# Optimization experiments

Hardware: AMD Instinct MI355X
Metric: run time of the kernel (lower is better)

Reference implementation:

```python
import jax, jax.numpy as jnp
import numpy as np

B = 256          # batch of molecules
N_ATOM = 1024    # atoms per molecule
N_EDGE = 8192    # directed edges per molecule (avg degree 8)
NEG_SLOPE = 0.01 # torch LeakyReLU default


def setup_inputs() -> dict:
    key = jax.random.key(0)
    ks = jax.random.split(key, 8)
    x = jax.random.normal(ks[0], (B, 3 * N_ATOM), dtype=jnp.float32)
    edge_index = jax.random.randint(ks[1], (2, N_EDGE), 0, N_ATOM, dtype=jnp.int64)
    # GCNConv weights (Glorot-ish small scale) and biases
    W1 = jax.random.normal(ks[2], (3, 64), dtype=jnp.float32) * 0.3
    b1 = jnp.zeros((64,), jnp.float32)
    W2 = jax.random.normal(ks[3], (64, 64), dtype=jnp.float32) * 0.1
    b2 = jnp.zeros((64,), jnp.float32)
    # project MLP: Linear(64,128) + LeakyReLU
    Wp = jax.random.normal(ks[4], (64, 128), dtype=jnp.float32) * 0.1
    bp = jnp.zeros((128,), jnp.float32)
    return {"x": x, "edge_index": edge_index, "W1": W1, "b1": b1,
            "W2": W2, "b2": b2, "Wp": Wp, "bp": bp}


def _leaky_relu(v):
    return jnp.where(v >= 0, v, NEG_SLOPE * v)


def reference(x, edge_index, W1, b1, W2, b2, Wp, bp):
    # x: [B, 3*n_atom] -> node features [B, n_atom, 3]
    bsz, n_feat = x.shape
    n = n_feat // 3
    h = x.reshape(bsz, n, 3)

    src = edge_index[0]  # message sources
    dst = edge_index[1]  # aggregation targets

    # GCN normalization with self-loops: deg[i] = 1 + in-degree(i)
    ones_e = jnp.ones((src.shape[0],), x.dtype)
    deg = jax.ops.segment_sum(ones_e, dst, num_segments=n) + 1.0
    dinv = jax.lax.rsqrt(deg)                # deg^{-1/2}, deg >= 1
    norm_e = dinv[src] * dinv[dst]           # [E]
    norm_self = dinv * dinv                  # self-loop weight per node

    def gcn(h, W, b):
        hw = h @ W                                        # [B, n, d_out]
        msg = hw[:, src, :] * norm_e[None, :, None]       # [B, E, d_out]
        agg = jax.vmap(lambda m: jax.ops.segment_sum(m, dst, num_segments=n))(msg)
        return agg + norm_self[None, :, None] * hw + b

    h = _leaky_relu(gcn(h, W1, b1))
    h = _leaky_relu(gcn(h, W2, b2))

    # global_mean_pool: every graph has exactly n atoms -> mean over atom axis
    g = h.mean(axis=1)                                    # [B, 64]

    # project MLP: Linear + LeakyReLU
    return _leaky_relu(g @ Wp + bp)                       # [B, 128]
```

## Files before the change

kernel.cpp:

```cpp
#include <hip/hip_runtime.h>

#define N_ATOMS 1024
#define N_EDGES 8192
#define NBATCH  256
#define NEG     0.01f

typedef unsigned int u32;
typedef __attribute__((ext_vector_type(2))) float f32x2;
typedef __attribute__((ext_vector_type(4))) float f32x4;
typedef __attribute__((ext_vector_type(8))) _Float16 f16x8;

__device__ __forceinline__ u32 pkrtz(float lo, float hi) {
    u32 r;
    asm("v_cvt_pkrtz_f16_f32 %0, %1, %2" : "=v"(r) : "v"(lo), "v"(hi));
    return r;
}
#define FMIX_LO(a, w, u) \
    asm("v_fma_mix_f32 %0, %1, %2, %0 op_sel_hi:[0,1,0]" : "+v"(a) : "v"(w), "v"(u))
#define FMIX_HI(a, w, u) \
    asm("v_fma_mix_f32 %0, %1, %2, %0 op_sel:[0,1,0] op_sel_hi:[0,1,0]" : "+v"(a) : "v"(w), "v"(u))

#define ROWPTR_OFF 0
#define COLW_OFF   4352
#define SELFW_OFF  (4352 + 73728)
#define PERM_OFF   (SELFW_OFF + 4096)
#define W2T_OFF    (PERM_OFF + 4096)

#define TSTR_B 144
#define SM_TILE_BYTES (N_ATOMS * TSTR_B)
#define SM_AUX_OFF SM_TILE_BYTES
#define SM_TOTAL (SM_TILE_BYTES + 12288)

__global__ __launch_bounds__(1024) void build_csr(
    const int* __restrict__ ei,
    int*  __restrict__ rowptr,
    int2* __restrict__ colw,
    float* __restrict__ selfw_g,
    int*  __restrict__ perm_g,
    u32*  __restrict__ w2t,
    const float* __restrict__ W2)
{
    __shared__ int   sdeg[N_ATOMS];
    __shared__ int   sstart[N_ATOMS];
    __shared__ float sdinv[N_ATOMS];
    __shared__ int   wtot[16];
    __shared__ int   hist[128];
    const int t = threadIdx.x;
    const int lane = t & 63;
    const int w = t >> 6;
    const int* srcA = ei;
    const int* dstA = ei + N_EDGES;

    sdeg[t] = 0;
    if (t < 128) hist[t] = 0;
    __syncthreads();
    for (int e = t; e < N_EDGES; e += 1024) atomicAdd(&sdeg[dstA[e]], 1);
    __syncthreads();

    const int deg  = sdeg[t];
    const int pdeg = (deg + 1) & ~1;
    int v = pdeg;
    #pragma unroll
    for (int d = 1; d < 64; d <<= 1) {
        int u = __shfl_up(v, d, 64);
        if (lane >= d) v += u;
    }
    if (lane == 63) wtot[w] = v;
    __syncthreads();
    if (t == 0) {
        int run = 0;
        #pragma unroll
        for (int i = 0; i < 16; ++i) { int c = wtot[i]; wtot[i] = run; run += c; }
    }
    __syncthreads();
    const int start = v - pdeg + wtot[w];
    sstart[t] = start;
    const float dv = rsqrtf((float)deg + 1.0f);
    sdinv[t] = dv;
    rowptr[t] = start;
    if (t == N_ATOMS - 1) rowptr[N_ATOMS] = start + pdeg;
    selfw_g[t] = dv * dv;
    if (deg & 1) colw[start + deg] = make_int2(0, 0);

    #pragma unroll
    for (int i = 0; i < 2; ++i) {
        const int idx = t + i * 1024;
        const int c = idx >> 5, kk = idx & 31;
        w2t[c * 32 + kk] = pkrtz(W2[(2 * kk) * 64 + c], W2[(2 * kk + 1) * 64 + c]);
    }

    const int dcl = deg < 127 ? deg : 127;
    atomicAdd(&hist[dcl], 1);
    sdeg[t] = 0;
    __syncthreads();
    if (t == 0) {
        int run = 0;
        for (int i = 0; i < 128; ++i) { int c = hist[i]; hist[i] = run; run += c; }
    }
    __syncthreads();
    const int pos = atomicAdd(&hist[dcl], 1);
    perm_g[pos] = t;
    __syncthreads();

    for (int e = t; e < N_EDGES; e += 1024) {
        const int d = dstA[e];
        const int s = srcA[e];
        const int slot = atomicAdd(&sdeg[d], 1);
        const float wgt = sdinv[s] * sdinv[d];
        colw[sstart[d] + slot] = make_int2(s, __float_as_int(wgt));
    }
}

#define FMIX_SET(q0, q1, q2, q3, wt)                                  \
    do {                                                              \
        FMIX_LO(acc[0],  wt, (q0).x); FMIX_HI(acc[1],  wt, (q0).x);   \
        FMIX_LO(acc[2],  wt, (q0).y); FMIX_HI(acc[3],  wt, (q0).y);   \
        FMIX_LO(acc[4],  wt, (q0).z); FMIX_HI(acc[5],  wt, (q0).z);   \
        FMIX_LO(acc[6],  wt, (q0).w); FMIX_HI(acc[7],  wt, (q0).w);   \
        FMIX_LO(acc[8],  wt, (q1).x); FMIX_HI(acc[9],  wt, (q1).x);   \
        FMIX_LO(acc[10], wt, (q1).y); FMIX_HI(acc[11], wt, (q1).y);   \
        FMIX_LO(acc[12], wt, (q1).z); FMIX_HI(acc[13], wt, (q1).z);   \
        FMIX_LO(acc[14], wt, (q1).w); FMIX_HI(acc[15], wt, (q1).w);   \
        FMIX_LO(acc[16], wt, (q2).x); FMIX_HI(acc[17], wt, (q2).x);   \
        FMIX_LO(acc[18], wt, (q2).y); FMIX_HI(acc[19], wt, (q2).y);   \
        FMIX_LO(acc[20], wt, (q2).z); FMIX_HI(acc[21], wt, (q2).z);   \
        FMIX_LO(acc[22], wt, (q2).w); FMIX_HI(acc[23], wt, (q2).w);   \
        FMIX_LO(acc[24], wt, (q3).x); FMIX_HI(acc[25], wt, (q3).x);   \
        FMIX_LO(acc[26], wt, (q3).y); FMIX_HI(acc[27], wt, (q3).y);   \
        FMIX_LO(acc[28], wt, (q3).z); FMIX_HI(acc[29], wt, (q3).z);   \
        FMIX_LO(acc[30], wt, (q3).w); FMIX_HI(acc[31], wt, (q3).w);   \
    } while (0)

#define LOAD_SET(q0, q1, q2, q3, rowbase)                 \
    do {                                                  \
        const uint4* _r = (const uint4*)(rowbase);        \
        q0 = _r[0]; q1 = _r[1]; q2 = _r[2]; q3 = _r[3];   \
    } while (0)

__global__ __launch_bounds__(1024, 4) void gnn_main(
    const float* __restrict__ x,
    const int*  __restrict__ rowptr,
    const int2* __restrict__ colw,
    const float* __restrict__ selfw_g,
    const int*  __restrict__ perm_g,
    const float* __restrict__ W1, const float* __restrict__ b1,
    const u32*  __restrict__ w2t, const float* __restrict__ b2,
    const float* __restrict__ Wp, const float* __restrict__ bp,
    float* __restrict__ out)
{
    extern __shared__ char smem[];
    float2* cx2 = (float2*)(smem + SM_AUX_OFF);
    float*  cz  = (float*)(smem + SM_AUX_OFF + 8192);
    float*  paux  = (float*)(smem + SM_AUX_OFF);
    float*  wpool = paux;
    float*  gvec  = paux + 1024;
    float*  proj  = paux + 1088;

    const int t = threadIdx.x;
    const int b = blockIdx.x;
    const float* xb = x + (size_t)b * (3 * N_ATOMS);

    const int ho   = (t & 1) * 64;
    const int pidx = t >> 1;

    const int atom1 = perm_g[t];
    const int s0p1  = rowptr[atom1];
    const int s1p1  = rowptr[atom1 + 1];
    const float swp1 = selfw_g[atom1];

    int atomR[2], s0R[2], neR[2];
    float swR[2];
    #pragma unroll
    for (int r = 0; r < 2; ++r) {
        const int a = perm_g[r * 512 + pidx];
        atomR[r] = a;
        s0R[r] = rowptr[a];
        neR[r] = rowptr[a + 1] - s0R[r];
        swR[r] = selfw_g[a];
    }

    {
        cx2[t] = make_float2(xb[3 * t], xb[3 * t + 1]);
        cz[t]  = xb[3 * t + 2];
    }
    __syncthreads();

    {
        const float2 cs = cx2[atom1];
        float A0 = swp1 * cs.x, A1 = swp1 * cs.y, A2 = swp1 * cz[atom1];
        int4 cur = make_int4(0, 0, 0, 0);
        if (s0p1 < s1p1) cur = *(const int4*)(colw + s0p1);
        for (int j = s0p1; j < s1p1; j += 2) {
            const int jn = (j + 2 < s1p1) ? (j + 2) : s0p1;
            const int4 nxt = *(const int4*)(colw + jn);
            const float2 c0 = cx2[cur.x];
            const float2 c1 = cx2[cur.z];
            const float z0 = cz[cur.x], z1 = cz[cur.z];
            const float w0 = __int_as_float(cur.y), w1 = __int_as_float(cur.w);
            A0 += w0 * c0.x + w1 * c1.x;
            A1 += w0 * c0.y + w1 * c1.y;
            A2 += w0 * z0 + w1 * z1;
            cur = nxt;
        }
        u32 pw[32];
        #pragma unroll
        for (int p = 0; p < 32; ++p) {
            f32x2 vv = *(const f32x2*)(b1 + 2 * p);
            vv = __builtin_elementwise_fma((f32x2){A0, A0}, *(const f32x2*)(W1 + 2 * p), vv);
            vv = __builtin_elementwise_fma((f32x2){A1, A1}, *(const f32x2*)(W1 + 64 + 2 * p), vv);
            vv = __builtin_elementwise_fma((f32x2){A2, A2}, *(const f32x2*)(W1 + 128 + 2 * p), vv);
            vv.x = fmaxf(vv.x, NEG * vv.x);
            vv.y = fmaxf(vv.y, NEG * vv.y);
            pw[p] = pkrtz(vv.x, vv.y);
        }
        uint4* trow = (uint4*)(smem + (size_t)atom1 * TSTR_B);
        #pragma unroll
        for (int q = 0; q < 8; ++q)
            trow[q] = make_uint4(pw[4 * q], pw[4 * q + 1], pw[4 * q + 2], pw[4 * q + 3]);
    }
    __syncthreads();

    u32 pr[2][16];
    #pragma unroll
    for (int r = 0; r < 2; ++r) {
        const int atom = atomR[r];
        const int s0e = s0R[r];
        const int ne  = neR[r];
        const float swk = swR[r];
        const int2* colw2 = (const int2*)(colw + s0e);

        float acc[32];
        #pragma unroll
        for (int f = 0; f < 32; ++f) acc[f] = 0.0f;
        {
            uint4 s0q, s1q, s2q, s3q;
            LOAD_SET(s0q, s1q, s2q, s3q, smem + (size_t)atom * TSTR_B + ho);
            FMIX_SET(s0q, s1q, s2q, s3q, swk);
        }
        if (ne > 0) {
            int2 cwA = colw2[0];
            uint4 a0, a1, a2, a3, b0, b1_, b2_, b3;
            LOAD_SET(a0, a1, a2, a3, smem + (size_t)cwA.x * TSTR_B + ho);
            for (int j = 0; j < ne; j += 2) {
                const int2 cwB = colw2[j + 1];
                LOAD_SET(b0, b1_, b2_, b3, smem + (size_t)cwB.x * TSTR_B + ho);
                FMIX_SET(a0, a1, a2, a3, __int_as_float(cwA.y));
                if (j + 2 < ne) {
                    cwA = colw2[j + 2];
                    LOAD_SET(a0, a1, a2, a3, smem + (size_t)cwA.x * TSTR_B + ho);
                }
                FMIX_SET(b0, b1_, b2_, b3, __int_as_float(cwB.y));
            }
        }
        #pragma unroll
        for (int i = 0; i < 16; ++i) pr[r][i] = pkrtz(acc[2 * i], acc[2 * i + 1]);
    }

    const int l15 = t & 15;
    const int lq  = (t & 63) >> 4;
    const int w   = t >> 6;
    f16x8 wf[2][4];
    #pragma unroll
    for (int kt = 0; kt < 2; ++kt)
        #pragma unroll
        for (int ct = 0; ct < 4; ++ct)
            wf[kt][ct] = *(const f16x8*)(w2t + (ct * 16 + l15) * 32 + kt * 16 + lq * 4);
    float bias[4];
    #pragma unroll
    for (int ct = 0; ct < 4; ++ct) bias[ct] = b2[ct * 16 + l15];

    __syncthreads();

    #pragma unroll
    for (int r = 0; r < 2; ++r) {
        uint4* dst = (uint4*)(smem + (size_t)atomR[r] * TSTR_B + ho);
        dst[0] = make_uint4(pr[r][0],  pr[r][1],  pr[r][2],  pr[r][3]);
        dst[1] = make_uint4(pr[r][4],  pr[r][5],  pr[r][6],  pr[r][7]);
        dst[2] = make_uint4(pr[r][8],  pr[r][9],  pr[r][10], pr[r][11]);
        dst[3] = make_uint4(pr[r][12], pr[r][13], pr[r][14], pr[r][15]);
    }

    {
        float pool[4] = {0.f, 0.f, 0.f, 0.f};
        #pragma unroll
        for (int rt = 0; rt < 4; ++rt) {
            const int po = (rt & 1) ? (16 + l15) : l15;
            const int arow = (rt < 2) ? __shfl(atomR[0], 2 * po, 64)
                                      : __shfl(atomR[1], 2 * po, 64);
            const char* ab = smem + (size_t)arow * TSTR_B + lq * 16;
            const f16x8 a0 = *(const f16x8*)(ab);
            const f16x8 a1 = *(const f16x8*)(ab + 64);
            #pragma unroll
            for (int ct = 0; ct < 4; ++ct) {
                f32x4 cf = {0.f, 0.f, 0.f, 0.f};
                cf = __builtin_amdgcn_mfma_f32_16x16x32_f16(a0, wf[0][ct], cf, 0, 0, 0);
                cf = __builtin_amdgcn_mfma_f32_16x16x32_f16(a1, wf[1][ct], cf, 0, 0, 0);
                float s = 0.0f;
                #pragma unroll
                for (int rr = 0; rr < 4; ++rr) {
                    const float vv = cf[rr] + bias[ct];
                    s += fmaxf(vv, NEG * vv);
                }
                pool[ct] += s;
            }
        }
        #pragma unroll
        for (int ct = 0; ct < 4; ++ct) {
            pool[ct] += __shfl_xor(pool[ct], 16, 64);
            pool[ct] += __shfl_xor(pool[ct], 32, 64);
        }
        if ((t & 63) < 16) {
            #pragma unroll
            for (int ct = 0; ct < 4; ++ct)
                wpool[w * 64 + ct * 16 + l15] = pool[ct];
        }
    }
    __syncthreads();

    if (t < 64) {
        float s = 0.0f;
        #pragma unroll
        for (int ww = 0; ww < 16; ++ww) s += wpool[ww * 64 + t];
        gvec[t] = s * (1.0f / 1024.0f);
    }
    __syncthreads();
    if (t < 512) {
        const int col = t & 127, pc = t >> 7;
        float s = 0.0f;
        #pragma unroll
        for (int f = 0; f < 16; ++f)
            s += gvec[pc * 16 + f] * Wp[(pc * 16 + f) * 128 + col];
        proj[pc * 128 + col] = s;
    }
    __syncthreads();
    if (t < 128) {
        float s = bp[t] + proj[t] + proj[128 + t] + proj[256 + t] + proj[384 + t];
        s = fmaxf(s, NEG * s);
        out[(size_t)b * 128 + t] = s;
    }
}

extern "C" void kernel_launch(void* const* d_in, const int* in_sizes, int n_in,
                              void* d_out, int out_size, void* d_ws, size_t ws_size,
                              hipStream_t stream) {
    const float* x  = (const float*)d_in[0];
    const int*   ei = (const int*)  d_in[1];
    const float* W1 = (const float*)d_in[2];
    const float* b1 = (const float*)d_in[3];
    const float* W2 = (const float*)d_in[4];
    const float* b2 = (const float*)d_in[5];
    const float* Wp = (const float*)d_in[6];
    const float* bp = (const float*)d_in[7];
    float* out = (float*)d_out;

    char* ws = (char*)d_ws;
    int*   rowptr = (int*)  (ws + ROWPTR_OFF);
    int2*  colw   = (int2*) (ws + COLW_OFF);
    float* selfw  = (float*)(ws + SELFW_OFF);
    int*   perm   = (int*)  (ws + PERM_OFF);
    u32*   w2t    = (u32*)  (ws + W2T_OFF);

    build_csr<<<1, 1024, 0, stream>>>(ei, rowptr, colw, selfw, perm, w2t, W2);

    (void)hipFuncSetAttribute((const void*)gnn_main,
                              hipFuncAttributeMaxDynamicSharedMemorySize, SM_TOTAL);
    gnn_main<<<NBATCH, 1024, SM_TOTAL, stream>>>(
        x, rowptr, colw, selfw, perm, W1, b1, w2t, b2, Wp, bp, out);
}
```

Before: 38.08 us.

## Fuse CSR construction into main GNN kernel with per-block redundant build

Removes the separate single-block build_csr launch. Each batch block now rebuilds the degree counts, CSR offsets, normalization weights and degree-sorted permutation itself in shared memory, and writes its own private copy of the edge list to global workspace. This eliminates the serial single-block prologue and the dependency between the two launches. In exchange every block repeats the edge-scanning and atomic work and writes its own edge array. W2 packing is also repeated by all blocks into one shared buffer, which is benign only because every block writes identical values.

```diff
diff --git a/kernel.cpp b/kernel.cpp
--- a/kernel.cpp
+++ b/kernel.cpp
@@ -20,96 +20,22 @@
 #define FMIX_HI(a, w, u) \
     asm("v_fma_mix_f32 %0, %1, %2, %0 op_sel:[0,1,0] op_sel_hi:[0,1,0]" : "+v"(a) : "v"(w), "v"(u))
 
-#define ROWPTR_OFF 0
-#define COLW_OFF   4352
-#define SELFW_OFF  (4352 + 73728)
-#define PERM_OFF   (SELFW_OFF + 4096)
-#define W2T_OFF    (PERM_OFF + 4096)
+#define W2T_OFF     0
+#define COLW_BASE   65536
+#define COLW_ENTS   9216
 
 #define TSTR_B 144
 #define SM_TILE_BYTES (N_ATOMS * TSTR_B)
 #define SM_AUX_OFF SM_TILE_BYTES
 #define SM_TOTAL (SM_TILE_BYTES + 12288)
 
-__global__ __launch_bounds__(1024) void build_csr(
-    const int* __restrict__ ei,
-    int*  __restrict__ rowptr,
-    int2* __restrict__ colw,
-    float* __restrict__ selfw_g,
-    int*  __restrict__ perm_g,
-    u32*  __restrict__ w2t,
-    const float* __restrict__ W2)
-{
-    __shared__ int   sdeg[N_ATOMS];
-    __shared__ int   sstart[N_ATOMS];
-    __shared__ float sdinv[N_ATOMS];
-    __shared__ int   wtot[16];
-    __shared__ int   hist[128];
-    const int t = threadIdx.x;
-    const int lane = t & 63;
-    const int w = t >> 6;
-    const int* srcA = ei;
-    const int* dstA = ei + N_EDGES;
-
-    sdeg[t] = 0;
-    if (t < 128) hist[t] = 0;
-    __syncthreads();
-    for (int e = t; e < N_EDGES; e += 1024) atomicAdd(&sdeg[dstA[e]], 1);
-    __syncthreads();
-
-    const int deg  = sdeg[t];
-    const int pdeg = (deg + 1) & ~1;
-    int v = pdeg;
-    #pragma unroll
-    for (int d = 1; d < 64; d <<= 1) {
-        int u = __shfl_up(v, d, 64);
-        if (lane >= d) v += u;
-    }
-    if (lane == 63) wtot[w] = v;
-    __syncthreads();
-    if (t == 0) {
-        int run = 0;
-        #pragma unroll
-        for (int i = 0; i < 16; ++i) { int c = wtot[i]; wtot[i] = run; run += c; }
-    }
-    __syncthreads();
-    const int start = v - pdeg + wtot[w];
-    sstart[t] = start;
-    const float dv = rsqrtf((float)deg + 1.0f);
-    sdinv[t] = dv;
-    rowptr[t] = start;
-    if (t == N_ATOMS - 1) rowptr[N_ATOMS] = start + pdeg;
-    selfw_g[t] = dv * dv;
-    if (deg & 1) colw[start + deg] = make_int2(0, 0);
-
-    #pragma unroll
-    for (int i = 0; i < 2; ++i) {
-        const int idx = t + i * 1024;
-        const int c = idx >> 5, kk = idx & 31;
-        w2t[c * 32 + kk] = pkrtz(W2[(2 * kk) * 64 + c], W2[(2 * kk + 1) * 64 + c]);
-    }
-
-    const int dcl = deg < 127 ? deg : 127;
-    atomicAdd(&hist[dcl], 1);
-    sdeg[t] = 0;
-    __syncthreads();
-    if (t == 0) {
-        int run = 0;
-        for (int i = 0; i < 128; ++i) { int c = hist[i]; hist[i] = run; run += c; }
-    }
-    __syncthreads();
-    const int pos = atomicAdd(&hist[dcl], 1);
-    perm_g[pos] = t;
-    __syncthreads();
-
-    for (int e = t; e < N_EDGES; e += 1024) {
-        const int d = dstA[e];
-        const int s = srcA[e];
-        const int slot = atomicAdd(&sdeg[d], 1);
-        const float wgt = sdinv[s] * sdinv[d];
-        colw[sstart[d] + slot] = make_int2(s, __float_as_int(wgt));
-    }
-}
+#define SC_SDEG   0
+#define SC_SSTART 4096
+#define SC_SDINV  8192
+#define SC_SPERM  12288
+#define SC_SPDEG  16384
+#define SC_WTOT   20480
+#define SC_HIST   20608
 
 #define FMIX_SET(q0, q1, q2, q3, wt)                                  \
     do {                                                              \
@@ -137,18 +63,24 @@
         q0 = _r[0]; q1 = _r[1]; q2 = _r[2]; q3 = _r[3];   \
     } while (0)
 
-__global__ __launch_bounds__(1024, 4) void gnn_main(
+__global__ __launch_bounds__(1024, 4) void gnn_all(
     const float* __restrict__ x,
-    const int*  __restrict__ rowptr,
-    const int2* __restrict__ colw,
-    const float* __restrict__ selfw_g,
-    const int*  __restrict__ perm_g,
+    const int*  __restrict__ ei,
     const float* __restrict__ W1, const float* __restrict__ b1,
-    const u32*  __restrict__ w2t, const float* __restrict__ b2,
+    const float* __restrict__ W2, const float* __restrict__ b2,
     const float* __restrict__ Wp, const float* __restrict__ bp,
+    int2* __restrict__ colw_all,
+    u32*  __restrict__ w2t,
     float* __restrict__ out)
 {
     extern __shared__ char smem[];
+    int*   sdeg   = (int*)  (smem + SC_SDEG);
+    int*   sstart = (int*)  (smem + SC_SSTART);
+    float* sdinv  = (float*)(smem + SC_SDINV);
+    int*   sperm  = (int*)  (smem + SC_SPERM);
+    int*   spdeg  = (int*)  (smem + SC_SPDEG);
+    int*   wtot   = (int*)  (smem + SC_WTOT);
+    int*   hist   = (int*)  (smem + SC_HIST);
     float2* cx2 = (float2*)(smem + SM_AUX_OFF);
     float*  cz  = (float*)(smem + SM_AUX_OFF + 8192);
     float*  paux  = (float*)(smem + SM_AUX_OFF);
@@ -158,28 +90,93 @@
 
     const int t = threadIdx.x;
     const int b = blockIdx.x;
-    const float* xb = x + (size_t)b * (3 * N_ATOMS);
+    const int lane = t & 63;
+    const int wv = t >> 6;
+    const int* srcA = ei;
+    const int* dstA = ei + N_EDGES;
+    int2* colw = colw_all + (size_t)b * COLW_ENTS;
+
+    sdeg[t] = 0;
+    if (t < 128) hist[t] = 0;
+    __syncthreads();
+    for (int e = t; e < N_EDGES; e += 1024) atomicAdd(&sdeg[dstA[e]], 1);
+    __syncthreads();
+
+    const int deg  = sdeg[t];
+    const int pdeg = (deg + 1) & ~1;
+    int v = pdeg;
+    #pragma unroll
+    for (int d = 1; d < 64; d <<= 1) {
+        int u = __shfl_up(v, d, 64);
+        if (lane >= d) v += u;
+    }
+    if (lane == 63) wtot[wv] = v;
+    __syncthreads();
+    if (t == 0) {
+        int run = 0;
+        #pragma unroll
+        for (int i = 0; i < 16; ++i) { int c = wtot[i]; wtot[i] = run; run += c; }
+    }
+    __syncthreads();
+    const int start = v - pdeg + wtot[wv];
+    sstart[t] = start;
+    spdeg[t]  = pdeg;
+    const float dv = rsqrtf((float)deg + 1.0f);
+    sdinv[t] = dv;
+    if (deg & 1) colw[start + deg] = make_int2(0, 0);
+
+    #pragma unroll
+    for (int i = 0; i < 2; ++i) {
+        const int idx = t + i * 1024;
+        const int c = idx >> 5, kk = idx & 31;
+        w2t[c * 32 + kk] = pkrtz(W2[(2 * kk) * 64 + c], W2[(2 * kk + 1) * 64 + c]);
+    }
+
+    const int dcl = deg < 127 ? deg : 127;
+    atomicAdd(&hist[dcl], 1);
+    sdeg[t] = 0;
+    __syncthreads();
+    if (t == 0) {
+        int run = 0;
+        for (int i = 0; i < 128; ++i) { int c = hist[i]; hist[i] = run; run += c; }
+    }
+    __syncthreads();
+    const int pos = atomicAdd(&hist[dcl], 1);
+    sperm[pos] = t;
+    __syncthreads();
+
+    for (int e = t; e < N_EDGES; e += 1024) {
+        const int d = dstA[e];
+        const int s = srcA[e];
+        const int slot = atomicAdd(&sdeg[d], 1);
+        const float wgt = sdinv[s] * sdinv[d];
+        colw[sstart[d] + slot] = make_int2(s, __float_as_int(wgt));
+    }
+    __syncthreads();
 
     const int ho   = (t & 1) * 64;
     const int pidx = t >> 1;
 
-    const int atom1 = perm_g[t];
-    const int s0p1  = rowptr[atom1];
-    const int s1p1  = rowptr[atom1 + 1];
-    const float swp1 = selfw_g[atom1];
+    const int atom1 = sperm[t];
+    const int s0p1  = sstart[atom1];
+    const int s1p1  = s0p1 + spdeg[atom1];
+    const float dv1 = sdinv[atom1];
+    const float swp1 = dv1 * dv1;
 
     int atomR[2], s0R[2], neR[2];
     float swR[2];
     #pragma unroll
     for (int r = 0; r < 2; ++r) {
-        const int a = perm_g[r * 512 + pidx];
+        const int a = sperm[r * 512 + pidx];
         atomR[r] = a;
-        s0R[r] = rowptr[a];
-        neR[r] = rowptr[a + 1] - s0R[r];
-        swR[r] = selfw_g[a];
+        s0R[r] = sstart[a];
+        neR[r] = spdeg[a];
+        const float d2 = sdinv[a];
+        swR[r] = d2 * d2;
     }
 
     {
+        const float* xb = x + (size_t)b * (3 * N_ATOMS);
         cx2[t] = make_float2(xb[3 * t], xb[3 * t + 1]);
         cz[t]  = xb[3 * t + 2];
     }
@@ -354,16 +351,11 @@
     float* out = (float*)d_out;
 
     char* ws = (char*)d_ws;
-    int*   rowptr = (int*)  (ws + ROWPTR_OFF);
-    int2*  colw   = (int2*) (ws + COLW_OFF);
-    float* selfw  = (float*)(ws + SELFW_OFF);
-    int*   perm   = (int*)  (ws + PERM_OFF);
-    u32*   w2t    = (u32*)  (ws + W2T_OFF);
-
-    build_csr<<<1, 1024, 0, stream>>>(ei, rowptr, colw, selfw, perm, w2t, W2);
-
-    (void)hipFuncSetAttribute((const void*)gnn_main,
+    u32*  w2t      = (u32*) (ws + W2T_OFF);
+    int2* colw_all = (int2*)(ws + COLW_BASE);
+
+    (void)hipFuncSetAttribute((const void*)gnn_all,
                               hipFuncAttributeMaxDynamicSharedMemorySize, SM_TOTAL);
-    gnn_main<<<NBATCH, 1024, SM_TOTAL, stream>>>(
-        x, rowptr, colw, selfw, perm, W1, b1, w2t, b2, Wp, bp, out);
+    gnn_all<<<NBATCH, 1024, SM_TOTAL, stream>>>(
+        x, ei, W1, b1, W2, b2, Wp, bp, colw_all, w2t, out);
 }
```

Result: slower. 40.86 us (+7.3%).
